# Kernel optimization log

Hardware: AMD Instinct MI355X
Metric: run time of the kernel (lower is better)

The kernel has to match this reference:

```python
import jax, jax.numpy as jnp
import numpy as np

N_FEATURES = 40
H = 64
N_CLASSES = 3
N_NODES = 100000
N_EDGES = 3200000
THRESHOLD = 0.5


def setup_inputs() -> dict:
    key = jax.random.key(0)
    ks = jax.random.split(key, 8)
    x = jax.random.normal(ks[0], (N_NODES, N_FEATURES), dtype=jnp.float32)
    edge_index = jax.random.randint(ks[1], (2, N_EDGES), 0, N_NODES, dtype=jnp.int64)
    s1 = 1.0 / np.sqrt(N_FEATURES)
    s2 = 1.0 / np.sqrt(H)
    W1 = jax.random.uniform(ks[2], (N_FEATURES, H), jnp.float32, -s1, s1)
    b1 = jnp.zeros((H,), jnp.float32)
    Wf = jax.random.uniform(ks[3], (H, H), jnp.float32, -s2, s2)
    bf = jax.random.uniform(ks[4], (H,), jnp.float32, -s2, s2)
    W2 = jax.random.uniform(ks[5], (H, N_CLASSES), jnp.float32, -s2, s2)
    b2 = jnp.zeros((N_CLASSES,), jnp.float32)
    ethical_filter = jnp.ones((N_CLASSES,), jnp.float32)
    return {"x": x, "edge_index": edge_index, "W1": W1, "b1": b1,
            "Wf": Wf, "bf": bf, "W2": W2, "b2": b2,
            "ethical_filter": ethical_filter}


def _gcn_conv(x, W, b, src, dst, n_nodes):
    # PyG GCNConv: add self-loops, symmetric normalization, src->dst aggregate.
    h = x @ W                                   # [N, F_out]
    loop = jnp.arange(n_nodes, dtype=src.dtype)
    s = jnp.concatenate([src, loop])            # [E+N]
    d = jnp.concatenate([dst, loop])
    deg = jnp.zeros((n_nodes,), h.dtype).at[d].add(1.0)
    dinv = jax.lax.rsqrt(deg)                   # deg >= 1 due to self-loops
    norm = dinv[s] * dinv[d]                    # [E+N]
    msg = h[s] * norm[:, None]                  # gather + scale
    out = jnp.zeros((n_nodes, h.shape[1]), h.dtype).at[d].add(msg)
    return out + b


def reference(x, edge_index, W1, b1, Wf, bf, W2, b2, ethical_filter):
    n = x.shape[0]
    src, dst = edge_index[0], edge_index[1]
    h = jax.nn.relu(_gcn_conv(x, W1, b1, src, dst, n))
    # SpikingNeuron: mem = fc(h); spike = (mem >= threshold).float()
    spike = (h @ Wf + bf >= THRESHOLD).astype(x.dtype)
    out = _gcn_conv(spike, W2, b2, src, dst, n)
    return out * ethical_filter
```

## Files before the change

### kernel.cpp

```cpp
#include <hip/hip_runtime.h>

#define NF 40
#define NF4 10
#define H  64
#define NC 3
#define BK 256
#define CAP 10240
#define MAXNBK 512
#define SMASK 0xFFFFFu
#define EPB 6400

__global__ void k_zero(int* __restrict__ p, int n) {
    int i = blockIdx.x * blockDim.x + threadIdx.x;
    if (i < n) p[i] = 0;
}

__global__ __launch_bounds__(512) void k_bin2(const int* __restrict__ src,
                                              const int* __restrict__ dst,
                                              int* __restrict__ gcur,
                                              unsigned* __restrict__ staging,
                                              int ne, int nbk) {
    __shared__ unsigned sorted[EPB];
    __shared__ unsigned short sbk[EPB];
    __shared__ int cnt[MAXNBK];
    __shared__ int tsum[MAXNBK];
    __shared__ int lstart[MAXNBK];
    __shared__ int gbase[MAXNBK];
    __shared__ int cur[MAXNBK];
    int t = threadIdx.x;
    int e0 = blockIdx.x * EPB;
    int m = min(EPB, ne - e0);
    if (m <= 0) return;

    for (int b = t; b < MAXNBK; b += 512) cnt[b] = 0;
    __syncthreads();
    for (int j = t; j < m; j += 512)
        atomicAdd(&cnt[dst[e0 + j] >> 8], 1);
    __syncthreads();
    int val = (t < nbk) ? cnt[t] : 0;
    tsum[t] = val;
    __syncthreads();
    for (int off = 1; off < 512; off <<= 1) {
        int a = (t >= off) ? tsum[t - off] : 0;
        __syncthreads();
        tsum[t] += a;
        __syncthreads();
    }
    lstart[t] = tsum[t] - val;
    cur[t] = tsum[t] - val;
    if (t < nbk) gbase[t] = val ? atomicAdd(&gcur[t], val) : 0;
    __syncthreads();
    for (int j = t; j < m; j += 512) {
        int d = dst[e0 + j], s = src[e0 + j];
        int b = d >> 8;
        int p = atomicAdd(&cur[b], 1);
        sorted[p] = ((unsigned)(d & 255) << 20) | (unsigned)s;
        sbk[p] = (unsigned short)b;
    }
    __syncthreads();
    for (int j = t; j < m; j += 512) {
        int b = sbk[j];
        staging[(size_t)b * CAP + gbase[b] + (j - lstart[b])] = sorted[j];
    }
}

__global__ __launch_bounds__(512) void k_sort(unsigned* __restrict__ staging,
                                              const int* __restrict__ gcur,
                                              int* __restrict__ rs, int* __restrict__ rl,
                                              float* __restrict__ dinv, int n) {
    __shared__ unsigned buf[CAP];
    __shared__ int cnt[BK];
    __shared__ int scn[BK];
    __shared__ int cur[BK];
    int b = blockIdx.x, t = threadIdx.x;
    int ebase = b * CAP;
    int rlen = gcur[b];
    for (int j = t; j < rlen; j += 512) buf[j] = staging[ebase + j];
    if (t < BK) cnt[t] = 0;
    __syncthreads();
    for (int j = t; j < rlen; j += 512)
        atomicAdd(&cnt[buf[j] >> 20], 1);
    __syncthreads();
    if (t < BK) scn[t] = cnt[t];
    __syncthreads();
    for (int off = 1; off < BK; off <<= 1) {
        int a = (t < BK && t >= off) ? scn[t - off] : 0;
        __syncthreads();
        if (t < BK) scn[t] += a;
        __syncthreads();
    }
    if (t < BK) {
        int deg = cnt[t];
        int excl = scn[t] - deg;
        cur[t] = excl;
        int node = b * BK + t;
        if (node < n) {
            rs[node] = ebase + excl;
            rl[node] = deg;
            dinv[node] = rsqrtf((float)(deg + 1));
        }
    }
    __syncthreads();
    for (int j = t; j < rlen; j += 512) {
        unsigned e = buf[j];
        int p = atomicAdd(&cur[e >> 20], 1);
        staging[ebase + p] = e;
    }
}

__global__ __launch_bounds__(256) void k_scale(const float4* __restrict__ x4,
                                               const float* __restrict__ dinv,
                                               float4* __restrict__ xs4, int total) {
    int i = blockIdx.x * blockDim.x + threadIdx.x;
    if (i < total) {
        float dd = dinv[i / NF4];
        float4 v = x4[i];
        xs4[i] = make_float4(v.x * dd, v.y * dd, v.z * dd, v.w * dd);
    }
}

__global__ __launch_bounds__(256) void k_pull1_xs(
        const unsigned* __restrict__ st, const int* __restrict__ rs,
        const int* __restrict__ rl, const float* __restrict__ dinv,
        const float4* __restrict__ xs4, float4* __restrict__ ax4, int n) {
    __shared__ float4 red[4][64];
    int t = threadIdx.x;
    int w = t >> 6, lane = t & 63;
    int d = blockIdx.x * 4 + w;
    if (d >= n) return;
    int g = lane / 10, f = lane - g * 10;
    int beg = rs[d], len = rl[d];
    float dd = dinv[d];
    float4 acc = make_float4(0.f, 0.f, 0.f, 0.f);
    if (g < 6) {
        int j = beg + g, end = beg + len;
        for (; j + 6 < end; j += 12) {
            unsigned eA = st[j], eB = st[j + 6];
            float4 a4 = xs4[(eA & SMASK) * NF4 + f];
            float4 b4 = xs4[(eB & SMASK) * NF4 + f];
            acc.x += a4.x + b4.x;
            acc.y += a4.y + b4.y;
            acc.z += a4.z + b4.z;
            acc.w += a4.w + b4.w;
        }
        if (j < end) {
            unsigned e = st[j];
            float4 v = xs4[(e & SMASK) * NF4 + f];
            acc.x += v.x; acc.y += v.y; acc.z += v.z; acc.w += v.w;
        }
    }
    red[w][lane] = acc;
    if (lane < NF4) {
        float4 tot = red[w][lane];
        #pragma unroll
        for (int gg = 1; gg < 6; ++gg) {
            float4 r = red[w][gg * 10 + lane];
            tot.x += r.x; tot.y += r.y; tot.z += r.z; tot.w += r.w;
        }
        float4 self = xs4[d * NF4 + lane];
        float4 o;
        o.x = dd * (tot.x + self.x);
        o.y = dd * (tot.y + self.y);
        o.z = dd * (tot.z + self.z);
        o.w = dd * (tot.w + self.w);
        ax4[d * NF4 + lane] = o;
    }
}

__global__ __launch_bounds__(256) void k_pull1_od(
        const unsigned* __restrict__ st, const int* __restrict__ rs,
        const int* __restrict__ rl, const float* __restrict__ dinv,
        const float4* __restrict__ x4, float4* __restrict__ ax4, int n) {
    __shared__ float4 red[4][64];
    int t = threadIdx.x;
    int w = t >> 6, lane = t & 63;
    int d = blockIdx.x * 4 + w;
    if (d >= n) return;
    int g = lane / 10, f = lane - g * 10;
    int beg = rs[d], len = rl[d];
    float dd = dinv[d];
    float4 acc = make_float4(0.f, 0.f, 0.f, 0.f);
    if (g < 6) {
        int j = beg + g, end = beg + len;
        for (; j + 6 < end; j += 12) {
            unsigned eA = st[j], eB = st[j + 6];
            int sA = (int)(eA & SMASK), sB = (int)(eB & SMASK);
            float wA = dinv[sA], wB = dinv[sB];
            float4 a4 = x4[sA * NF4 + f];
            float4 b4 = x4[sB * NF4 + f];
            acc.x += a4.x * wA + b4.x * wB;
            acc.y += a4.y * wA + b4.y * wB;
            acc.z += a4.z * wA + b4.z * wB;
            acc.w += a4.w * wA + b4.w * wB;
        }
        if (j < end) {
            unsigned e = st[j];
            int s = (int)(e & SMASK);
            float wv = dinv[s];
            float4 v = x4[s * NF4 + f];
            acc.x += v.x * wv; acc.y += v.y * wv;
            acc.z += v.z * wv; acc.w += v.w * wv;
        }
    }
    red[w][lane] = acc;
    if (lane < NF4) {
        float4 tot = red[w][lane];
        #pragma unroll
        for (int gg = 1; gg < 6; ++gg) {
            float4 r = red[w][gg * 10 + lane];
            tot.x += r.x; tot.y += r.y; tot.z += r.z; tot.w += r.w;
        }
        float4 self = x4[d * NF4 + lane];
        float4 o;
        o.x = dd * (tot.x + self.x * dd);
        o.y = dd * (tot.y + self.y * dd);
        o.z = dd * (tot.z + self.z * dd);
        o.w = dd * (tot.w + self.w * dd);
        ax4[d * NF4 + lane] = o;
    }
}

__global__ __launch_bounds__(256, 2) void k_node(
        const float4* __restrict__ ax4,
        const float* __restrict__ W1, const float* __restrict__ b1,
        const float* __restrict__ Wf, const float* __restrict__ bf,
        const float* __restrict__ W2, const float* __restrict__ dinv,
        float4* __restrict__ s2sp4, int n) {
    __shared__ float lW1[NF * H];
    __shared__ float lWf[H * H];
    __shared__ float hT[4][H * 32];
    int t = threadIdx.x, w = t >> 6, lane = t & 63;
    int r = lane & 7, c = lane >> 3;

    for (int i = t; i < NF * H; i += 256) lW1[i] = W1[i];
    for (int i = t; i < H * H;  i += 256) lWf[i] = Wf[i];
    __syncthreads();

    int nb0 = (blockIdx.x * 4 + w) * 32;
    if (nb0 >= n) return;
    int cnt = min(32, n - nb0);

    float bb[8], bfv[8], w2s[8][3];
    #pragma unroll
    for (int j = 0; j < 8; ++j) {
        bb[j]  = b1[8 * c + j];
        bfv[j] = bf[8 * c + j];
        w2s[j][0] = W2[(8 * c + j) * NC + 0];
        w2s[j][1] = W2[(8 * c + j) * NC + 1];
        w2s[j][2] = W2[(8 * c + j) * NC + 2];
    }

    float* axT = &hT[w][0];
    #pragma unroll
    for (int i = 0; i < 5; ++i) {
        int idx = lane + 64 * i;
        int no = idx / NF4, q = idx - no * NF4;
        float4 a = make_float4(0.f, 0.f, 0.f, 0.f);
        if (no < cnt) a = ax4[(size_t)(nb0 + no) * NF4 + q];
        axT[(4 * q + 0) * 32 + no] = a.x;
        axT[(4 * q + 1) * 32 + no] = a.y;
        axT[(4 * q + 2) * 32 + no] = a.z;
        axT[(4 * q + 3) * 32 + no] = a.w;
    }

    float acc[4][8];
    #pragma unroll
    for (int i = 0; i < 4; ++i)
        #pragma unroll
        for (int j = 0; j < 8; ++j) acc[i][j] = bb[j];
    for (int k = 0; k < NF; ++k) {
        float4 a   = *(const float4*)&axT[k * 32 + 4 * r];
        float4 blo = *(const float4*)&lW1[k * H + 8 * c];
        float4 bhi = *(const float4*)&lW1[k * H + 8 * c + 4];
        float av[4] = {a.x, a.y, a.z, a.w};
        float bv[8] = {blo.x, blo.y, blo.z, blo.w, bhi.x, bhi.y, bhi.z, bhi.w};
        #pragma unroll
        for (int i = 0; i < 4; ++i)
            #pragma unroll
            for (int j = 0; j < 8; ++j) acc[i][j] = fmaf(av[i], bv[j], acc[i][j]);
    }
    #pragma unroll
    for (int j = 0; j < 8; ++j) {
        float4 hv = make_float4(fmaxf(acc[0][j], 0.f), fmaxf(acc[1][j], 0.f),
                                fmaxf(acc[2][j], 0.f), fmaxf(acc[3][j], 0.f));
        *(float4*)&hT[w][(8 * c + j) * 32 + 4 * r] = hv;
    }

    float acc2[4][8];
    #pragma unroll
    for (int i = 0; i < 4; ++i)
        #pragma unroll
        for (int j = 0; j < 8; ++j) acc2[i][j] = bfv[j];
    for (int k = 0; k < H; ++k) {
        float4 a   = *(const float4*)&hT[w][k * 32 + 4 * r];
        float4 blo = *(const float4*)&lWf[k * H + 8 * c];
        float4 bhi = *(const float4*)&lWf[k * H + 8 * c + 4];
        float av[4] = {a.x, a.y, a.z, a.w};
        float bv[8] = {blo.x, blo.y, blo.z, blo.w, bhi.x, bhi.y, bhi.z, bhi.w};
        #pragma unroll
        for (int i = 0; i < 4; ++i)
            #pragma unroll
            for (int j = 0; j < 8; ++j) acc2[i][j] = fmaf(av[i], bv[j], acc2[i][j]);
    }

    float p0[4], p1[4], p2[4];
    #pragma unroll
    for (int i = 0; i < 4; ++i) { p0[i] = 0.f; p1[i] = 0.f; p2[i] = 0.f; }
    #pragma unroll
    for (int i = 0; i < 4; ++i)
        #pragma unroll
        for (int j = 0; j < 8; ++j) {
            float s = (acc2[i][j] >= 0.5f) ? 1.f : 0.f;
            p0[i] = fmaf(s, w2s[j][0], p0[i]);
            p1[i] = fmaf(s, w2s[j][1], p1[i]);
            p2[i] = fmaf(s, w2s[j][2], p2[i]);
        }
    #pragma unroll
    for (int off = 8; off < 64; off <<= 1) {
        #pragma unroll
        for (int i = 0; i < 4; ++i) {
            p0[i] += __shfl_xor(p0[i], off);
            p1[i] += __shfl_xor(p1[i], off);
            p2[i] += __shfl_xor(p2[i], off);
        }
    }
    if (c == 0) {
        #pragma unroll
        for (int i = 0; i < 4; ++i) {
            int no = 4 * r + i;
            if (no < cnt) {
                int node = nb0 + no;
                float di = dinv[node];
                s2sp4[node] = make_float4(p0[i] * di, p1[i] * di, p2[i] * di, 0.f);
            }
        }
    }
}

__global__ __launch_bounds__(256) void k_pull2(
        const unsigned* __restrict__ st, const int* __restrict__ rs,
        const int* __restrict__ rl, const float* __restrict__ dinv,
        const float4* __restrict__ s2sp4, const float* __restrict__ b2,
        const float* __restrict__ ef, float* __restrict__ out, int n) {
    int t = threadIdx.x;
    int w = t >> 6, lane = t & 63;
    int d = blockIdx.x * 4 + w;
    if (d >= n) return;
    int beg = rs[d], end = beg + rl[d];
    float a0 = 0.f, a1 = 0.f, a2 = 0.f;
    for (int j = beg + lane; j < end; j += 64) {
        float4 v = s2sp4[st[j] & SMASK];
        a0 += v.x; a1 += v.y; a2 += v.z;
    }
    for (int off = 32; off; off >>= 1) {
        a0 += __shfl_down(a0, off);
        a1 += __shfl_down(a1, off);
        a2 += __shfl_down(a2, off);
    }
    if (lane == 0) {
        float dd = dinv[d];
        float4 self = s2sp4[d];
        out[d * NC + 0] = (dd * (a0 + self.x) + b2[0]) * ef[0];
        out[d * NC + 1] = (dd * (a1 + self.y) + b2[1]) * ef[1];
        out[d * NC + 2] = (dd * (a2 + self.z) + b2[2]) * ef[2];
    }
}

extern "C" void kernel_launch(void* const* d_in, const int* in_sizes, int n_in,
                              void* d_out, int out_size, void* d_ws, size_t ws_size,
                              hipStream_t stream) {
    const float* x  = (const float*)d_in[0];
    const int*   ei = (const int*)d_in[1];
    const float* W1 = (const float*)d_in[2];
    const float* b1 = (const float*)d_in[3];
    const float* Wf = (const float*)d_in[4];
    const float* bf = (const float*)d_in[5];
    const float* W2 = (const float*)d_in[6];
    const float* b2 = (const float*)d_in[7];
    const float* ef = (const float*)d_in[8];

    int n  = in_sizes[0] / NF;
    int ne = in_sizes[1] / 2;
    const int* src = ei;
    const int* dst = ei + ne;
    int nbk = (n + BK - 1) >> 8;

    auto al = [](size_t v) { return (v + 255) & ~(size_t)255; };
    char* ws = (char*)d_ws;
    size_t off = 0;
    unsigned* staging = (unsigned*)(ws + off); off += al((size_t)nbk * CAP * 4);
    float*    axbuf   = (float*)(ws + off);    off += al((size_t)n * NF * 4);
    float*    s2sp    = (float*)(ws + off);    off += al((size_t)n * 4 * 4);
    float*    dinv    = (float*)(ws + off);    off += al((size_t)n * 4);
    int*      rsb     = (int*)(ws + off);      off += al((size_t)n * 4);
    int*      rlb     = (int*)(ws + off);      off += al((size_t)n * 4);
    int*      gcur    = (int*)(ws + off);      off += al((size_t)MAXNBK * 4);
    float*    xsbuf   = (float*)(ws + off);
    size_t    need_xs = off + al((size_t)n * NF * 4);
    bool use_xs = (ws_size >= need_xs);
    float* out = (float*)d_out;

    int binblocks = (ne + EPB - 1) / EPB;

    k_zero <<<2, 256, 0, stream>>>(gcur, MAXNBK);
    k_bin2 <<<binblocks, 512, 0, stream>>>(src, dst, gcur, staging, ne, nbk);
    k_sort <<<nbk, 512, 0, stream>>>(staging, gcur, rsb, rlb, dinv, n);
    if (use_xs) {
        k_scale  <<<(n * NF4 + 255) / 256, 256, 0, stream>>>((const float4*)x, dinv,
                                                             (float4*)xsbuf, n * NF4);
        k_pull1_xs<<<(n + 3) / 4, 256, 0, stream>>>(staging, rsb, rlb, dinv,
                                                    (const float4*)xsbuf,
                                                    (float4*)axbuf, n);
    } else {
        k_pull1_od<<<(n + 3) / 4, 256, 0, stream>>>(staging, rsb, rlb, dinv,
                                                    (const float4*)x, (float4*)axbuf, n);
    }
    k_node <<<(n + 127) / 128, 256, 0, stream>>>(
        (const float4*)axbuf, W1, b1, Wf, bf, W2, dinv, (float4*)s2sp, n);
    k_pull2<<<(n + 3) / 4, 256, 0, stream>>>(staging, rsb, rlb, dinv, (const float4*)s2sp,
                                             b2, ef, out, n);
}
```

Before: 217.0 us.

## Slice neighbor lists by source range and sweep slices grid-wide for cache locality

The sort now orders each destination's edges by destination and then by one of 8 source-index slices, and records per-node slice offsets. A new persistent layer-1 aggregation kernel walks all nodes slice by slice, with a spin-based grid soft barrier between slices, so the gathered feature rows at any moment come from a narrow source range that can stay resident in cache. It adds a per-node offset array, extra sort counters, and inter-block spin barriers with a bounded timeout. It also assumes all 1024 blocks are co-resident and each thread handles at most three nodes.

```diff
diff --git a/kernel.cpp b/kernel.cpp
--- a/kernel.cpp
+++ b/kernel.cpp
@@ -9,6 +9,9 @@
 #define MAXNBK 512
 #define SMASK 0xFFFFFu
 #define EPB 6400
+#define NSL 8
+#define SSH 14
+#define SPIN 150
 
 __global__ void k_zero(int* __restrict__ p, int n) {
     int i = blockIdx.x * blockDim.x + threadIdx.x;
@@ -67,43 +70,60 @@
 __global__ __launch_bounds__(512) void k_sort(unsigned* __restrict__ staging,
                                               const int* __restrict__ gcur,
                                               int* __restrict__ rs, int* __restrict__ rl,
-                                              float* __restrict__ dinv, int n) {
+                                              float* __restrict__ dinv,
+                                              int* __restrict__ sseg, int n) {
     __shared__ unsigned buf[CAP];
-    __shared__ int cnt[BK];
-    __shared__ int scn[BK];
-    __shared__ int cur[BK];
+    __shared__ int cnt[BK * NSL];
+    __shared__ int tsum[512];
     int b = blockIdx.x, t = threadIdx.x;
     int ebase = b * CAP;
     int rlen = gcur[b];
     for (int j = t; j < rlen; j += 512) buf[j] = staging[ebase + j];
-    if (t < BK) cnt[t] = 0;
-    __syncthreads();
-    for (int j = t; j < rlen; j += 512)
-        atomicAdd(&cnt[buf[j] >> 20], 1);
-    __syncthreads();
-    if (t < BK) scn[t] = cnt[t];
-    __syncthreads();
-    for (int off = 1; off < BK; off <<= 1) {
-        int a = (t < BK && t >= off) ? scn[t - off] : 0;
+    for (int i = t; i < BK * NSL; i += 512) cnt[i] = 0;
+    __syncthreads();
+    for (int j = t; j < rlen; j += 512) {
+        unsigned e = buf[j];
+        int key = (int)((e >> 20) * NSL) + (int)((e & SMASK) >> SSH);
+        atomicAdd(&cnt[key], 1);
+    }
+    __syncthreads();
+    int base4 = t * 4;
+    int loc[4]; int run = 0;
+    #pragma unroll
+    for (int i = 0; i < 4; ++i) { loc[i] = run; run += cnt[base4 + i]; }
+    tsum[t] = run;
+    __syncthreads();
+    for (int off = 1; off < 512; off <<= 1) {
+        int a = (t >= off) ? tsum[t - off] : 0;
         __syncthreads();
-        if (t < BK) scn[t] += a;
+        tsum[t] += a;
         __syncthreads();
     }
+    int texcl = tsum[t] - run;
+    #pragma unroll
+    for (int i = 0; i < 4; ++i) cnt[base4 + i] = texcl + loc[i];
+    __syncthreads();
     if (t < BK) {
-        int deg = cnt[t];
-        int excl = scn[t] - deg;
-        cur[t] = excl;
         int node = b * BK + t;
+        int st0 = cnt[t * NSL];
+        int en0 = (t == BK - 1) ? rlen : cnt[(t + 1) * NSL];
+        int deg = en0 - st0;
         if (node < n) {
-            rs[node] = ebase + excl;
+            rs[node] = ebase + st0;
             rl[node] = deg;
             dinv[node] = rsqrtf((float)(deg + 1));
+            if (sseg) {
+                #pragma unroll
+                for (int s = 0; s < NSL; ++s)
+                    sseg[(size_t)node * NSL + s] = ebase + cnt[t * NSL + s];
+            }
         }
     }
     __syncthreads();
     for (int j = t; j < rlen; j += 512) {
         unsigned e = buf[j];
-        int p = atomicAdd(&cur[e >> 20], 1);
+        int key = (int)((e >> 20) * NSL) + (int)((e & SMASK) >> SSH);
+        int p = atomicAdd(&cnt[key], 1);
         staging[ebase + p] = e;
     }
 }
@@ -116,6 +136,80 @@
         float dd = dinv[i / NF4];
         float4 v = x4[i];
         xs4[i] = make_float4(v.x * dd, v.y * dd, v.z * dd, v.w * dd);
+    }
+}
+
+__device__ __forceinline__ void soft_barrier(int* c, int target) {
+    __syncthreads();
+    if (threadIdx.x == 0) {
+        atomicAdd(c, 1);
+        for (int i = 0; i < SPIN; ++i) {
+            if (atomicAdd(c, 0) >= target) break;
+            __builtin_amdgcn_s_sleep(2);
+        }
+    }
+    __syncthreads();
+}
+
+__global__ __launch_bounds__(512, 8) void k_pull1_coop(
+        const unsigned* __restrict__ st, const int* __restrict__ sseg,
+        const int* __restrict__ rs, const int* __restrict__ rl,
+        const float* __restrict__ dinv, const float4* __restrict__ xs4,
+        float4* __restrict__ ax4, int* __restrict__ barr, int n) {
+    int t = threadIdx.x;
+    int wv = t >> 6, lane = t & 63;
+    int grp = lane / 10, f = lane - grp * 10;
+    bool act = (grp < 6);
+    int G = (blockIdx.x * 8 + wv) * 6 + (act ? grp : 0);
+    int NG = gridDim.x * 48;
+    int tgt = gridDim.x;
+
+    float4 a0 = make_float4(0.f, 0.f, 0.f, 0.f);
+    float4 a1 = make_float4(0.f, 0.f, 0.f, 0.f);
+    float4 a2 = make_float4(0.f, 0.f, 0.f, 0.f);
+    int n0 = G, n1 = G + NG, n2 = G + 2 * NG;
+    bool v0 = act && (n0 < n), v1 = act && (n1 < n), v2 = act && (n2 < n);
+
+    for (int sl = 0; sl < NSL; ++sl) {
+        #pragma unroll
+        for (int q = 0; q < 3; ++q) {
+            bool vq = (q == 0) ? v0 : (q == 1) ? v1 : v2;
+            if (!vq) continue;
+            int nd = (q == 0) ? n0 : (q == 1) ? n1 : n2;
+            int beg = sseg[(size_t)nd * NSL + sl];
+            int end = (sl == NSL - 1) ? rs[nd] + rl[nd]
+                                      : sseg[(size_t)nd * NSL + sl + 1];
+            float4 acc = (q == 0) ? a0 : (q == 1) ? a1 : a2;
+            int j = beg;
+            for (; j + 1 < end; j += 2) {
+                unsigned eA = st[j], eB = st[j + 1];
+                float4 xa = xs4[(eA & SMASK) * NF4 + f];
+                float4 xb = xs4[(eB & SMASK) * NF4 + f];
+                acc.x += xa.x + xb.x; acc.y += xa.y + xb.y;
+                acc.z += xa.z + xb.z; acc.w += xa.w + xb.w;
+            }
+            if (j < end) {
+                float4 xv = xs4[(st[j] & SMASK) * NF4 + f];
+                acc.x += xv.x; acc.y += xv.y; acc.z += xv.z; acc.w += xv.w;
+            }
+            if (q == 0) a0 = acc; else if (q == 1) a1 = acc; else a2 = acc;
+        }
+        if (sl < NSL - 1) soft_barrier(barr + sl, tgt);
+    }
+    #pragma unroll
+    for (int q = 0; q < 3; ++q) {
+        bool vq = (q == 0) ? v0 : (q == 1) ? v1 : v2;
+        if (!vq) continue;
+        int nd = (q == 0) ? n0 : (q == 1) ? n1 : n2;
+        float4 acc = (q == 0) ? a0 : (q == 1) ? a1 : a2;
+        float dd = dinv[nd];
+        float4 self = xs4[nd * NF4 + f];
+        float4 o;
+        o.x = dd * (acc.x + self.x);
+        o.y = dd * (acc.y + self.y);
+        o.z = dd * (acc.z + self.z);
+        o.w = dd * (acc.w + self.w);
+        ax4[(size_t)nd * NF4 + f] = o;
     }
 }
 
@@ -138,14 +232,11 @@
             unsigned eA = st[j], eB = st[j + 6];
             float4 a4 = xs4[(eA & SMASK) * NF4 + f];
             float4 b4 = xs4[(eB & SMASK) * NF4 + f];
-            acc.x += a4.x + b4.x;
-            acc.y += a4.y + b4.y;
-            acc.z += a4.z + b4.z;
-            acc.w += a4.w + b4.w;
+            acc.x += a4.x + b4.x; acc.y += a4.y + b4.y;
+            acc.z += a4.z + b4.z; acc.w += a4.w + b4.w;
         }
         if (j < end) {
-            unsigned e = st[j];
-            float4 v = xs4[(e & SMASK) * NF4 + f];
+            float4 v = xs4[(st[j] & SMASK) * NF4 + f];
             acc.x += v.x; acc.y += v.y; acc.z += v.z; acc.w += v.w;
         }
     }
@@ -394,18 +485,29 @@
     float*    dinv    = (float*)(ws + off);    off += al((size_t)n * 4);
     int*      rsb     = (int*)(ws + off);      off += al((size_t)n * 4);
     int*      rlb     = (int*)(ws + off);      off += al((size_t)n * 4);
-    int*      gcur    = (int*)(ws + off);      off += al((size_t)MAXNBK * 4);
+    int*      gcur    = (int*)(ws + off);      off += al((size_t)(MAXNBK + NSL) * 4);
+    int*      barr    = gcur + MAXNBK;
     float*    xsbuf   = (float*)(ws + off);
     size_t    need_xs = off + al((size_t)n * NF * 4);
-    bool use_xs = (ws_size >= need_xs);
+    int*      ssegb   = (int*)(ws + need_xs);
+    size_t    need_cp = need_xs + al((size_t)n * NSL * 4);
+    bool use_xs   = (ws_size >= need_xs);
+    bool use_coop = (ws_size >= need_cp);
     float* out = (float*)d_out;
 
     int binblocks = (ne + EPB - 1) / EPB;
 
-    k_zero <<<2, 256, 0, stream>>>(gcur, MAXNBK);
+    k_zero <<<(MAXNBK + NSL + 255) / 256, 256, 0, stream>>>(gcur, MAXNBK + NSL);
     k_bin2 <<<binblocks, 512, 0, stream>>>(src, dst, gcur, staging, ne, nbk);
-    k_sort <<<nbk, 512, 0, stream>>>(staging, gcur, rsb, rlb, dinv, n);
-    if (use_xs) {
+    k_sort <<<nbk, 512, 0, stream>>>(staging, gcur, rsb, rlb, dinv,
+                                     use_coop ? ssegb : (int*)nullptr, n);
+    if (use_coop) {
+        k_scale     <<<(n * NF4 + 255) / 256, 256, 0, stream>>>((const float4*)x, dinv,
+                                                                (float4*)xsbuf, n * NF4);
+        k_pull1_coop<<<1024, 512, 0, stream>>>(staging, ssegb, rsb, rlb, dinv,
+                                               (const float4*)xsbuf, (float4*)axbuf,
+                                               barr, n);
+    } else if (use_xs) {
         k_scale  <<<(n * NF4 + 255) / 256, 256, 0, stream>>>((const float4*)x, dinv,
                                                              (float4*)xsbuf, n * NF4);
         k_pull1_xs<<<(n + 3) / 4, 256, 0, stream>>>(staging, rsb, rlb, dinv,
```

Measured after the change: 559.8 us. 2.58x slower.
